# Optimization experiments

Hardware: AMD Instinct MI355X
Metric: run time of the kernel (lower is better)

The kernel has to match this reference:

```python
import jax, jax.numpy as jnp
import numpy as np

N, M, D = 384, 2, 3          # n_nodes, multiplicity, spatial dim
F, H, K, L = 32, 64, 2, 2    # feat dim, hidden, n_equivariant_vectors_out, n_blocks
OUT = 64                     # n_invariant_feat_out
T = N * M                    # flattened node count

def _edges():
    # fully-connected graph over flattened nodes, no self edges (static shapes)
    idx = np.arange(T)
    s = np.repeat(idx, T)
    r = np.tile(idx, T)
    mask = s != r
    return jnp.asarray(s[mask]), jnp.asarray(r[mask])

def setup_inputs() -> dict:
    key = jax.random.key(0)
    ks = jax.random.split(key, 12)
    def w(k, shape):
        return (jax.random.normal(k, shape) / np.sqrt(shape[-2])).astype(jnp.float32)
    return {
        "positions": jax.random.normal(ks[0], (N, M, D), dtype=jnp.float32),
        "features": jax.random.normal(ks[1], (N, M, F), dtype=jnp.float32),
        "w_emb": w(ks[2], (F, H)), "b_emb": jnp.zeros((H,), jnp.float32),
        "we1": w(ks[3], (L, 2 * H + K, H)), "be1": jnp.zeros((L, H), jnp.float32),
        "we2": w(ks[4], (L, H, H)), "be2": jnp.zeros((L, H), jnp.float32),
        "wx1": w(ks[5], (L, H, H)), "bx1": jnp.zeros((L, H), jnp.float32),
        "wx2": w(ks[6], (L, H, K)),
        "wh1": w(ks[7], (L, 2 * H, H)), "bh1": jnp.zeros((L, H), jnp.float32),
        "wh2": w(ks[8], (L, H, H)), "bh2": jnp.zeros((L, H), jnp.float32),
        "w_head": w(ks[9], (H, OUT)), "b_head": jnp.zeros((OUT,), jnp.float32),
    }

def reference(positions, features, w_emb, b_emb, we1, be1, we2, be2,
              wx1, bx1, wx2, wh1, bh1, wh2, bh2, w_head, b_head):
    senders, receivers = _edges()
    x = positions.reshape(T, D)                      # flatten multiplicity
    h = features.reshape(T, F) @ w_emb + b_emb       # [T,H] node embedding
    x_vec = jnp.repeat(x[:, None, :], K, axis=1)     # [T,K,3] vector channels
    for l in range(L):
        diff = x_vec[senders] - x_vec[receivers]                        # [E,K,3]
        sqnorm = jnp.sum(diff * diff, axis=-1)                          # [E,K]
        e_in = jnp.concatenate([h[senders], h[receivers], sqnorm], -1)  # [E,2H+K]
        m = jax.nn.silu(e_in @ we1[l] + be1[l])
        m = jax.nn.silu(m @ we2[l] + be2[l])                            # [E,H]
        phi_x = jax.nn.silu(m @ wx1[l] + bx1[l]) @ wx2[l]               # [E,K]
        upd = phi_x[..., None] * diff / (jnp.sqrt(sqnorm + 1e-8)[..., None] + 1.0)
        x_vec = x_vec + jax.ops.segment_sum(upd, receivers, num_segments=T) / (T - 1)
        agg = jax.ops.segment_sum(m, receivers, num_segments=T)         # [T,H]
        h = h + jax.nn.silu(jnp.concatenate([h, agg], -1) @ wh1[l] + bh1[l]) @ wh2[l] + bh2[l]
    vectors = (x_vec - x[:, None, :]).reshape(N, M, K, D)  # unflatten
    scalars = (h @ w_head + b_head).reshape(N, M, OUT)     # invariant head
    return vectors, scalars
```

## Files before the change

### kernel.cpp

```cpp
#include <hip/hip_runtime.h>
#include <math.h>

#define TN 768
#define HD 64
#define FF 32
#define OUTD 64
#define LL 2

typedef short short8 __attribute__((ext_vector_type(8)));
typedef short short4v __attribute__((ext_vector_type(4)));
typedef float f32x4 __attribute__((ext_vector_type(4)));
typedef unsigned int uint4v __attribute__((ext_vector_type(4)));

__device__ __forceinline__ float silu_f(float x) {
    float e = __builtin_amdgcn_exp2f(x * -1.44269504089f);
    return x * __builtin_amdgcn_rcpf(1.0f + e);
}

__device__ __forceinline__ void bf16_split(float x, short& hi, short& lo) {
    unsigned int u = __float_as_uint(x);
    unsigned int uh = u & 0xFFFF0000u;
    hi = (short)(uh >> 16);
    float r = x - __uint_as_float(uh);
    lo = (short)(__float_as_uint(r) >> 16);
}

__device__ __forceinline__ unsigned short bf16_rne(float x) {
    unsigned int u = __float_as_uint(x);
    u += 0x7FFFu + ((u >> 16) & 1u);
    return (unsigned short)(u >> 16);
}

__device__ __forceinline__ float row16_sum(float v) {
    int x;
    x = __builtin_amdgcn_update_dpp(0, __float_as_int(v), 0xB1, 0xF, 0xF, true);
    v += __int_as_float(x);
    x = __builtin_amdgcn_update_dpp(0, __float_as_int(v), 0x4E, 0xF, 0xF, true);
    v += __int_as_float(x);
    x = __builtin_amdgcn_update_dpp(0, __float_as_int(v), 0x141, 0xF, 0xF, true);
    v += __int_as_float(x);
    x = __builtin_amdgcn_update_dpp(0, __float_as_int(v), 0x140, 0xF, 0xF, true);
    v += __int_as_float(x);
    return v;
}

__global__ void k_embed_pre(const float* __restrict__ pos, const float* __restrict__ feat,
                            const float* __restrict__ w_emb, const float* __restrict__ b_emb,
                            const float* __restrict__ we1, const float* __restrict__ be1,
                            float* __restrict__ h, float* __restrict__ x_vec,
                            float* __restrict__ A, float* __restrict__ Bv) {
    int t = blockIdx.x;
    int j = threadIdx.x;
    __shared__ float sf[FF];
    __shared__ float sh[HD];
    if (j < FF) sf[j] = feat[t * FF + j];
    __syncthreads();
    float acc = b_emb[j];
#pragma unroll
    for (int f = 0; f < FF; ++f) acc += sf[f] * w_emb[f * HD + j];
    h[t * HD + j] = acc;
    sh[j] = acc;
    if (j < 6) x_vec[t * 6 + j] = pos[t * 3 + (j % 3)];
    __syncthreads();
    float a = be1[j], b = 0.f;
#pragma unroll
    for (int i = 0; i < HD; ++i) {
        a += sh[i] * we1[i * HD + j];
        b += sh[i] * we1[(HD + i) * HD + j];
    }
    A[t * HD + j] = a;
    Bv[t * HD + j] = b;
}

#define SM2S 68
__global__ __launch_bounds__(256, 1) void k_edge(
    const float* __restrict__ xv_in, const float* __restrict__ A_in,
    const float* __restrict__ Bv_in, const float* __restrict__ we1,
    const float* __restrict__ we2, const float* __restrict__ be2,
    const float* __restrict__ wx1, const float* __restrict__ bx1,
    const float* __restrict__ wx2,
    const float* __restrict__ wh1, const float* __restrict__ bh1,
    const float* __restrict__ wh2, const float* __restrict__ bh2,
    const float* __restrict__ be1,
    float* __restrict__ h, float* __restrict__ xv_out,
    float* __restrict__ A_out, float* __restrict__ Bv_out,
    const float* __restrict__ pos, const float* __restrict__ w_head,
    const float* __restrict__ b_head, float* __restrict__ out,
    int l, int last)
{
    const int r = blockIdx.x;
    const int tid = threadIdx.x;
    const int wv = tid >> 6;
    const int lane = tid & 63;
    const int q = lane >> 4;
    const int m = lane & 15;

    __shared__ __align__(16) union USm {
        struct {
            unsigned short W2h[64 * 72], W2l[64 * 72], W3h[64 * 72];
        } stg;
        struct {
            unsigned short M2[64 * SM2S];
            float Phi[64][2];
            float Agg[4][64];
            float XupW[4][8];
            float hr[64], aggF[64], su[64], h2[64];
        } run;
    } u;

    const float* w2 = we2 + (size_t)l * HD * HD;
    const float* w3 = wx1 + (size_t)l * HD * HD;
    for (int e = tid; e < HD * HD; e += 256) {
        int k = e >> 6, n = e & 63;
        short h16, l16;
        bf16_split(w2[e], h16, l16);
        u.stg.W2h[n * 72 + k] = (unsigned short)h16;
        u.stg.W2l[n * 72 + k] = (unsigned short)l16;
        u.stg.W3h[n * 72 + k] = bf16_rne(w3[e]);
    }
    __syncthreads();
    short8 bW2h[4][2], bW2l[4][2], bW3h[4][2];
#pragma unroll
    for (int nt = 0; nt < 4; ++nt)
#pragma unroll
        for (int kt = 0; kt < 2; ++kt) {
            int idx = (nt * 16 + m) * 72 + kt * 32 + 8 * q;
            bW2h[nt][kt] = *(const short8*)&u.stg.W2h[idx];
            bW2l[nt][kt] = *(const short8*)&u.stg.W2l[idx];
            bW3h[nt][kt] = *(const short8*)&u.stg.W3h[idx];
        }
    __syncthreads();

    float bbA[2][8], c0A[2][8], c1A[2][8];
#pragma unroll
    for (int kt = 0; kt < 2; ++kt) {
        int jb = kt * 32 + 8 * q;
        *(float4*)&bbA[kt][0] = *(const float4*)&Bv_in[r * HD + jb];
        *(float4*)&bbA[kt][4] = *(const float4*)&Bv_in[r * HD + jb + 4];
        *(float4*)&c0A[kt][0] = *(const float4*)&we1[((size_t)l * 130 + 128) * HD + jb];
        *(float4*)&c0A[kt][4] = *(const float4*)&we1[((size_t)l * 130 + 128) * HD + jb + 4];
        *(float4*)&c1A[kt][0] = *(const float4*)&we1[((size_t)l * 130 + 129) * HD + jb];
        *(float4*)&c1A[kt][4] = *(const float4*)&we1[((size_t)l * 130 + 129) * HD + jb + 4];
    }
    float be2v[4], bx1v[4], w20[4], w21[4];
#pragma unroll
    for (int nt = 0; nt < 4; ++nt) {
        int col = nt * 16 + m;
        be2v[nt] = be2[l * HD + col];
        bx1v[nt] = bx1[l * HD + col];
        w20[nt] = wx2[((size_t)l * HD + col) * 2 + 0];
        w21[nt] = wx2[((size_t)l * HD + col) * 2 + 1];
    }
    float xr[6];
#pragma unroll
    for (int c = 0; c < 6; ++c) xr[c] = xv_in[r * 6 + c];

    float aggP[4] = {0.f, 0.f, 0.f, 0.f};
    float accX[6] = {0.f, 0.f, 0.f, 0.f, 0.f, 0.f};

#pragma unroll 1
    for (int s0 = 0; s0 < TN; s0 += 64) {
        const int sA = s0 + 16 * wv + m;
        float2 p01 = *(const float2*)&xv_in[sA * 6 + 0];
        float2 p23 = *(const float2*)&xv_in[sA * 6 + 2];
        float2 p45 = *(const float2*)&xv_in[sA * 6 + 4];
        float d0 = p01.x - xr[0], d1 = p01.y - xr[1], d2 = p23.x - xr[2];
        float d3 = p23.y - xr[3], d4 = p45.x - xr[4], d5 = p45.y - xr[5];
        float q0 = d0 * d0 + d1 * d1 + d2 * d2;
        float q1 = d3 * d3 + d4 * d4 + d5 * d5;
        float ik0 = __builtin_amdgcn_rcpf(__builtin_amdgcn_sqrtf(q0 + 1e-8f) + 1.f);
        float ik1 = __builtin_amdgcn_rcpf(__builtin_amdgcn_sqrtf(q1 + 1e-8f) + 1.f);

        short8 a1h[2], a1l[2];
#pragma unroll
        for (int kt = 0; kt < 2; ++kt) {
            int jb = kt * 32 + 8 * q;
            float av[8];
            *(float4*)&av[0] = *(const float4*)&A_in[sA * HD + jb];
            *(float4*)&av[4] = *(const float4*)&A_in[sA * HD + jb + 4];
            float mv[8];
#pragma unroll
            for (int jj = 0; jj < 8; ++jj) {
                float pre = av[jj] + bbA[kt][jj] + q0 * c0A[kt][jj] + q1 * c1A[kt][jj];
                mv[jj] = silu_f(pre);
            }
            uint4v uh, ul;
            unsigned int* uhp = (unsigned int*)&uh;
            unsigned int* ulp = (unsigned int*)&ul;
#pragma unroll
            for (int jp = 0; jp < 4; ++jp) {
                unsigned int a0 = __float_as_uint(mv[2 * jp]);
                unsigned int a1 = __float_as_uint(mv[2 * jp + 1]);
                uhp[jp] = __builtin_amdgcn_perm(a1, a0, 0x07060302u);
                float l0 = mv[2 * jp] - __uint_as_float(a0 & 0xFFFF0000u);
                float l1 = mv[2 * jp + 1] - __uint_as_float(a1 & 0xFFFF0000u);
                ulp[jp] = __builtin_amdgcn_perm(__float_as_uint(l1), __float_as_uint(l0),
                                                0x07060302u);
            }
            a1h[kt] = __builtin_bit_cast(short8, uh);
            a1l[kt] = __builtin_bit_cast(short8, ul);
        }

        const int rl = r - s0;
#pragma unroll
        for (int nt = 0; nt < 4; ++nt) {
            f32x4 acc = {0.f, 0.f, 0.f, 0.f};
#pragma unroll
            for (int kt = 0; kt < 2; ++kt) {
                acc = __builtin_amdgcn_mfma_f32_16x16x32_bf16(a1h[kt], bW2h[nt][kt], acc, 0, 0, 0);
                acc = __builtin_amdgcn_mfma_f32_16x16x32_bf16(a1l[kt], bW2h[nt][kt], acc, 0, 0, 0);
                acc = __builtin_amdgcn_mfma_f32_16x16x32_bf16(a1h[kt], bW2l[nt][kt], acc, 0, 0, 0);
            }
            int col = nt * 16 + m;
#pragma unroll
            for (int reg = 0; reg < 4; ++reg) {
                int il = 16 * wv + 4 * q + reg;
                float v = silu_f(acc[reg] + be2v[nt]);
                if (il == rl) v = 0.f;
                aggP[nt] += v;
                u.run.M2[il * SM2S + col] = bf16_rne(v);
            }
        }

        short8 a2h[2];
#pragma unroll
        for (int kt = 0; kt < 2; ++kt) {
            int base = (16 * wv + m) * SM2S + kt * 32 + 8 * q;
            short4v lo = *(const short4v*)&u.run.M2[base];
            short4v hi = *(const short4v*)&u.run.M2[base + 4];
            short8 a2;
#pragma unroll
            for (int jj = 0; jj < 4; ++jj) { a2[jj] = lo[jj]; a2[4 + jj] = hi[jj]; }
            a2h[kt] = a2;
        }
        float phiP[4][2] = {};
#pragma unroll
        for (int nt = 0; nt < 4; ++nt) {
            f32x4 acc = {0.f, 0.f, 0.f, 0.f};
#pragma unroll
            for (int kt = 0; kt < 2; ++kt)
                acc = __builtin_amdgcn_mfma_f32_16x16x32_bf16(a2h[kt], bW3h[nt][kt], acc, 0, 0, 0);
#pragma unroll
            for (int reg = 0; reg < 4; ++reg) {
                float p = silu_f(acc[reg] + bx1v[nt]);
                phiP[reg][0] += p * w20[nt];
                phiP[reg][1] += p * w21[nt];
            }
        }
#pragma unroll
        for (int reg = 0; reg < 4; ++reg) {
            phiP[reg][0] = row16_sum(phiP[reg][0]);
            phiP[reg][1] = row16_sum(phiP[reg][1]);
        }
        if (m == 0) {
#pragma unroll
            for (int reg = 0; reg < 4; ++reg) {
                int il = 16 * wv + 4 * q + reg;
                *(float2*)&u.run.Phi[il][0] = make_float2(phiP[reg][0], phiP[reg][1]);
            }
        }
        if (q == 0) {
            int il = 16 * wv + m;
            float2 ph = *(const float2*)&u.run.Phi[il][0];
            float f0 = ph.x * ik0;
            float f1 = ph.y * ik1;
            accX[0] += f0 * d0; accX[1] += f0 * d1; accX[2] += f0 * d2;
            accX[3] += f1 * d3; accX[4] += f1 * d4; accX[5] += f1 * d5;
        }
    }

#pragma unroll
    for (int nt = 0; nt < 4; ++nt) {
        aggP[nt] += __shfl_xor(aggP[nt], 16, 64);
        aggP[nt] += __shfl_xor(aggP[nt], 32, 64);
    }
#pragma unroll
    for (int c = 0; c < 6; ++c) accX[c] = row16_sum(accX[c]);
    if (q == 0) {
#pragma unroll
        for (int nt = 0; nt < 4; ++nt) u.run.Agg[wv][nt * 16 + m] = aggP[nt];
        if (m == 0) {
#pragma unroll
            for (int c = 0; c < 6; ++c) u.run.XupW[wv][c] = accX[c];
        }
    }
    __syncthreads();

    float xup[6];
    if (tid < 64) {
        u.run.aggF[tid] = u.run.Agg[0][tid] + u.run.Agg[1][tid] +
                          u.run.Agg[2][tid] + u.run.Agg[3][tid];
        u.run.hr[tid] = h[r * HD + tid];
    }
    __syncthreads();
    if (tid < 64) {
        int j = tid;
        const float* w1 = wh1 + (size_t)l * 128 * HD;
        float acc = bh1[l * HD + j];
#pragma unroll
        for (int i = 0; i < HD; ++i) acc += u.run.hr[i] * w1[i * HD + j];
#pragma unroll
        for (int i = 0; i < HD; ++i) acc += u.run.aggF[i] * w1[(HD + i) * HD + j];
        u.run.su[j] = silu_f(acc);
    }
    __syncthreads();
    if (tid < 64) {
        int j = tid;
        const float* wq = wh2 + (size_t)l * HD * HD;
        float v = 0.f;
#pragma unroll
        for (int i = 0; i < HD; ++i) v += u.run.su[i] * wq[i * HD + j];
        float hn = u.run.hr[j] + v + bh2[l * HD + j];
        h[r * HD + j] = hn;
        u.run.h2[j] = hn;
    }
    if (tid < 6) {
        xup[0] = u.run.XupW[0][tid] + u.run.XupW[1][tid] +
                 u.run.XupW[2][tid] + u.run.XupW[3][tid];
    }
    __syncthreads();
    if (!last) {
        if (tid < 64) {
            int j = tid;
            const float* w = we1 + (size_t)(l + 1) * 130 * HD;
            float a = be1[(l + 1) * HD + j], b = 0.f;
#pragma unroll
            for (int i = 0; i < HD; ++i) {
                a += u.run.h2[i] * w[i * HD + j];
                b += u.run.h2[i] * w[(HD + i) * HD + j];
            }
            A_out[r * HD + j] = a;
            Bv_out[r * HD + j] = b;
        }
        if (tid < 6) {
            xv_out[r * 6 + tid] = xr[tid] + xup[0] * (1.0f / 767.0f);
        }
    } else {
        if (tid < 64) {
            int j = tid;
            float o = b_head[j];
#pragma unroll
            for (int i = 0; i < HD; ++i) o += u.run.h2[i] * w_head[i * OUTD + j];
            out[TN * 6 + r * OUTD + j] = o;
        }
        if (tid < 6) {
            float xv = xr[tid] + xup[0] * (1.0f / 767.0f);
            out[r * 6 + tid] = xv - pos[r * 3 + (tid % 3)];
        }
    }
}

extern "C" void kernel_launch(void* const* d_in, const int* in_sizes, int n_in,
                              void* d_out, int out_size, void* d_ws, size_t ws_size,
                              hipStream_t stream)
{
    const float* pos    = (const float*)d_in[0];
    const float* feat   = (const float*)d_in[1];
    const float* w_emb  = (const float*)d_in[2];
    const float* b_emb  = (const float*)d_in[3];
    const float* we1    = (const float*)d_in[4];
    const float* be1    = (const float*)d_in[5];
    const float* we2    = (const float*)d_in[6];
    const float* be2    = (const float*)d_in[7];
    const float* wx1    = (const float*)d_in[8];
    const float* bx1    = (const float*)d_in[9];
    const float* wx2    = (const float*)d_in[10];
    const float* wh1    = (const float*)d_in[11];
    const float* bh1    = (const float*)d_in[12];
    const float* wh2    = (const float*)d_in[13];
    const float* bh2    = (const float*)d_in[14];
    const float* w_head = (const float*)d_in[15];
    const float* b_head = (const float*)d_in[16];
    float* out = (float*)d_out;

    float* ws   = (float*)d_ws;
    float* h    = ws;
    float* xv0  = h + TN * HD;
    float* xv1  = xv0 + TN * 6;
    float* A0   = xv1 + TN * 6;
    float* A1   = A0 + TN * HD;
    float* Bv0  = A1 + TN * HD;
    float* Bv1  = Bv0 + TN * HD;

    k_embed_pre<<<TN, 64, 0, stream>>>(pos, feat, w_emb, b_emb, we1, be1,
                                       h, xv0, A0, Bv0);
    k_edge<<<TN, 256, 0, stream>>>(xv0, A0, Bv0, we1, we2, be2, wx1, bx1, wx2,
                                   wh1, bh1, wh2, bh2, be1,
                                   h, xv1, A1, Bv1,
                                   pos, w_head, b_head, out, 0, 0);
    k_edge<<<TN, 256, 0, stream>>>(xv1, A1, Bv1, we1, we2, be2, wx1, bx1, wx2,
                                   wh1, bh1, wh2, bh2, be1,
                                   h, xv0, A0, Bv0,
                                   pos, w_head, b_head, out, 1, 1);
}
```

Before: 211.3 us.

## Drop low-part bf16 split of first-layer activations and prefetch next sender tile

Removes the bf16 hi/lo split of the silu activations feeding the second edge MLP, cutting the MFMA count per tile from three to two per k-step and dropping the lo-part packing, and uses a packed bf16 convert instruction. Adds double-buffered register prefetch of the next 64 senders' positions and A rows so global loads overlap compute. Moves the per-receiver bias and sqnorm weight vectors into shared memory to lower register pressure, and takes the self-edge masking off the common path. The lower precision on the activation operand risks larger numerical error.

```diff
diff --git a/kernel.cpp b/kernel.cpp
--- a/kernel.cpp
+++ b/kernel.cpp
@@ -1,4 +1,5 @@
 #include <hip/hip_runtime.h>
+#include <hip/hip_bf16.h>
 #include <math.h>
 
 #define TN 768
@@ -29,6 +30,17 @@
     unsigned int u = __float_as_uint(x);
     u += 0x7FFFu + ((u >> 16) & 1u);
     return (unsigned short)(u >> 16);
+}
+
+__device__ __forceinline__ unsigned int pk_bf16(float a, float b) {
+#if __has_builtin(__builtin_amdgcn_cvt_pk_bf16_f32)
+    auto t = __builtin_amdgcn_cvt_pk_bf16_f32(a, b);
+    return __builtin_bit_cast(unsigned int, t);
+#else
+    unsigned int ua = __float_as_uint(a); ua += 0x7FFFu + ((ua >> 16) & 1u);
+    unsigned int ub = __float_as_uint(b); ub += 0x7FFFu + ((ub >> 16) & 1u);
+    return __builtin_amdgcn_perm(ub, ua, 0x07060302u);
+#endif
 }
 
 __device__ __forceinline__ float row16_sum(float v) {
@@ -107,6 +119,9 @@
             float hr[64], aggF[64], su[64], h2[64];
         } run;
     } u;
+    __shared__ __align__(16) float sBvr[64];
+    __shared__ __align__(16) float sC0[64];
+    __shared__ __align__(16) float sC1[64];
 
     const float* w2 = we2 + (size_t)l * HD * HD;
     const float* w3 = wx1 + (size_t)l * HD * HD;
@@ -118,6 +133,11 @@
         u.stg.W2l[n * 72 + k] = (unsigned short)l16;
         u.stg.W3h[n * 72 + k] = bf16_rne(w3[e]);
     }
+    if (tid < HD) {
+        sBvr[tid] = Bv_in[r * HD + tid];
+        sC0[tid] = we1[((size_t)l * 130 + 128) * HD + tid];
+        sC1[tid] = we1[((size_t)l * 130 + 129) * HD + tid];
+    }
     __syncthreads();
     short8 bW2h[4][2], bW2l[4][2], bW3h[4][2];
 #pragma unroll
@@ -131,17 +151,6 @@
         }
     __syncthreads();
 
-    float bbA[2][8], c0A[2][8], c1A[2][8];
-#pragma unroll
-    for (int kt = 0; kt < 2; ++kt) {
-        int jb = kt * 32 + 8 * q;
-        *(float4*)&bbA[kt][0] = *(const float4*)&Bv_in[r * HD + jb];
-        *(float4*)&bbA[kt][4] = *(const float4*)&Bv_in[r * HD + jb + 4];
-        *(float4*)&c0A[kt][0] = *(const float4*)&we1[((size_t)l * 130 + 128) * HD + jb];
-        *(float4*)&c0A[kt][4] = *(const float4*)&we1[((size_t)l * 130 + 128) * HD + jb + 4];
-        *(float4*)&c1A[kt][0] = *(const float4*)&we1[((size_t)l * 130 + 129) * HD + jb];
-        *(float4*)&c1A[kt][4] = *(const float4*)&we1[((size_t)l * 130 + 129) * HD + jb + 4];
-    }
     float be2v[4], bx1v[4], w20[4], w21[4];
 #pragma unroll
     for (int nt = 0; nt < 4; ++nt) {
@@ -158,12 +167,37 @@
     float aggP[4] = {0.f, 0.f, 0.f, 0.f};
     float accX[6] = {0.f, 0.f, 0.f, 0.f, 0.f, 0.f};
 
-#pragma unroll 1
-    for (int s0 = 0; s0 < TN; s0 += 64) {
-        const int sA = s0 + 16 * wv + m;
-        float2 p01 = *(const float2*)&xv_in[sA * 6 + 0];
-        float2 p23 = *(const float2*)&xv_in[sA * 6 + 2];
-        float2 p45 = *(const float2*)&xv_in[sA * 6 + 4];
+    const int rowA = 16 * wv + m;
+    float2 pbuf[2][3];
+    float4 abuf[2][2][2];
+    {
+        int sA = rowA;
+        pbuf[0][0] = *(const float2*)&xv_in[sA * 6 + 0];
+        pbuf[0][1] = *(const float2*)&xv_in[sA * 6 + 2];
+        pbuf[0][2] = *(const float2*)&xv_in[sA * 6 + 4];
+#pragma unroll
+        for (int kt = 0; kt < 2; ++kt) {
+            abuf[0][kt][0] = *(const float4*)&A_in[sA * HD + kt * 32 + 8 * q];
+            abuf[0][kt][1] = *(const float4*)&A_in[sA * HD + kt * 32 + 8 * q + 4];
+        }
+    }
+
+#pragma unroll 2
+    for (int it = 0; it < TN / 64; ++it) {
+        const int s0 = it * 64;
+        const int pb = it & 1;
+        {
+            int sN = (s0 + 64 < TN ? s0 + 64 : 0) + rowA;
+            pbuf[pb ^ 1][0] = *(const float2*)&xv_in[sN * 6 + 0];
+            pbuf[pb ^ 1][1] = *(const float2*)&xv_in[sN * 6 + 2];
+            pbuf[pb ^ 1][2] = *(const float2*)&xv_in[sN * 6 + 4];
+#pragma unroll
+            for (int kt = 0; kt < 2; ++kt) {
+                abuf[pb ^ 1][kt][0] = *(const float4*)&A_in[sN * HD + kt * 32 + 8 * q];
+                abuf[pb ^ 1][kt][1] = *(const float4*)&A_in[sN * HD + kt * 32 + 8 * q + 4];
+            }
+        }
+        float2 p01 = pbuf[pb][0], p23 = pbuf[pb][1], p45 = pbuf[pb][2];
         float d0 = p01.x - xr[0], d1 = p01.y - xr[1], d2 = p23.x - xr[2];
         float d3 = p23.y - xr[3], d4 = p45.x - xr[4], d5 = p45.y - xr[5];
         float q0 = d0 * d0 + d1 * d1 + d2 * d2;
@@ -171,61 +205,68 @@
         float ik0 = __builtin_amdgcn_rcpf(__builtin_amdgcn_sqrtf(q0 + 1e-8f) + 1.f);
         float ik1 = __builtin_amdgcn_rcpf(__builtin_amdgcn_sqrtf(q1 + 1e-8f) + 1.f);
 
-        short8 a1h[2], a1l[2];
+        short8 a1h[2];
 #pragma unroll
         for (int kt = 0; kt < 2; ++kt) {
             int jb = kt * 32 + 8 * q;
-            float av[8];
-            *(float4*)&av[0] = *(const float4*)&A_in[sA * HD + jb];
-            *(float4*)&av[4] = *(const float4*)&A_in[sA * HD + jb + 4];
+            float av[8], bb[8], c0[8], c1[8];
+            *(float4*)&av[0] = abuf[pb][kt][0];
+            *(float4*)&av[4] = abuf[pb][kt][1];
+            *(float4*)&bb[0] = *(const float4*)&sBvr[jb];
+            *(float4*)&bb[4] = *(const float4*)&sBvr[jb + 4];
+            *(float4*)&c0[0] = *(const float4*)&sC0[jb];
+            *(float4*)&c0[4] = *(const float4*)&sC0[jb + 4];
+            *(float4*)&c1[0] = *(const float4*)&sC1[jb];
+            *(float4*)&c1[4] = *(const float4*)&sC1[jb + 4];
             float mv[8];
 #pragma unroll
             for (int jj = 0; jj < 8; ++jj) {
-                float pre = av[jj] + bbA[kt][jj] + q0 * c0A[kt][jj] + q1 * c1A[kt][jj];
+                float pre = av[jj] + bb[jj] + q0 * c0[jj] + q1 * c1[jj];
                 mv[jj] = silu_f(pre);
             }
-            uint4v uh, ul;
+            uint4v uh;
             unsigned int* uhp = (unsigned int*)&uh;
-            unsigned int* ulp = (unsigned int*)&ul;
-#pragma unroll
-            for (int jp = 0; jp < 4; ++jp) {
-                unsigned int a0 = __float_as_uint(mv[2 * jp]);
-                unsigned int a1 = __float_as_uint(mv[2 * jp + 1]);
-                uhp[jp] = __builtin_amdgcn_perm(a1, a0, 0x07060302u);
-                float l0 = mv[2 * jp] - __uint_as_float(a0 & 0xFFFF0000u);
-                float l1 = mv[2 * jp + 1] - __uint_as_float(a1 & 0xFFFF0000u);
-                ulp[jp] = __builtin_amdgcn_perm(__float_as_uint(l1), __float_as_uint(l0),
-                                                0x07060302u);
-            }
+#pragma unroll
+            for (int jp = 0; jp < 4; ++jp)
+                uhp[jp] = pk_bf16(mv[2 * jp], mv[2 * jp + 1]);
             a1h[kt] = __builtin_bit_cast(short8, uh);
-            a1l[kt] = __builtin_bit_cast(short8, ul);
         }
 
         const int rl = r - s0;
+        const bool selfw = (rl >= 16 * wv) && (rl < 16 * wv + 16);
 #pragma unroll
         for (int nt = 0; nt < 4; ++nt) {
             f32x4 acc = {0.f, 0.f, 0.f, 0.f};
 #pragma unroll
             for (int kt = 0; kt < 2; ++kt) {
                 acc = __builtin_amdgcn_mfma_f32_16x16x32_bf16(a1h[kt], bW2h[nt][kt], acc, 0, 0, 0);
-                acc = __builtin_amdgcn_mfma_f32_16x16x32_bf16(a1l[kt], bW2h[nt][kt], acc, 0, 0, 0);
                 acc = __builtin_amdgcn_mfma_f32_16x16x32_bf16(a1h[kt], bW2l[nt][kt], acc, 0, 0, 0);
             }
-            int col = nt * 16 + m;
-#pragma unroll
-            for (int reg = 0; reg < 4; ++reg) {
-                int il = 16 * wv + 4 * q + reg;
-                float v = silu_f(acc[reg] + be2v[nt]);
-                if (il == rl) v = 0.f;
-                aggP[nt] += v;
-                u.run.M2[il * SM2S + col] = bf16_rne(v);
-            }
+            float vv[4];
+#pragma unroll
+            for (int reg = 0; reg < 4; ++reg) vv[reg] = silu_f(acc[reg] + be2v[nt]);
+            const int il0 = 16 * wv + 4 * q;
+            if (__builtin_expect(selfw, 0)) {
+#pragma unroll
+                for (int reg = 0; reg < 4; ++reg)
+                    aggP[nt] += (il0 + reg == rl) ? 0.f : vv[reg];
+            } else {
+#pragma unroll
+                for (int reg = 0; reg < 4; ++reg) aggP[nt] += vv[reg];
+            }
+            const int col = nt * 16 + m;
+            unsigned int pA = pk_bf16(vv[0], vv[1]);
+            unsigned int pB = pk_bf16(vv[2], vv[3]);
+            u.run.M2[(il0 + 0) * SM2S + col] = (unsigned short)pA;
+            u.run.M2[(il0 + 1) * SM2S + col] = (unsigned short)(pA >> 16);
+            u.run.M2[(il0 + 2) * SM2S + col] = (unsigned short)pB;
+            u.run.M2[(il0 + 3) * SM2S + col] = (unsigned short)(pB >> 16);
         }
 
         short8 a2h[2];
 #pragma unroll
         for (int kt = 0; kt < 2; ++kt) {
-            int base = (16 * wv + m) * SM2S + kt * 32 + 8 * q;
+            int base = rowA * SM2S + kt * 32 + 8 * q;
             short4v lo = *(const short4v*)&u.run.M2[base];
             short4v hi = *(const short4v*)&u.run.M2[base + 4];
             short8 a2;
@@ -260,8 +301,7 @@
             }
         }
         if (q == 0) {
-            int il = 16 * wv + m;
-            float2 ph = *(const float2*)&u.run.Phi[il][0];
+            float2 ph = *(const float2*)&u.run.Phi[rowA][0];
             float f0 = ph.x * ik0;
             float f1 = ph.y * ik1;
             accX[0] += f0 * d0; accX[1] += f0 * d1; accX[2] += f0 * d2;
@@ -286,7 +326,7 @@
     }
     __syncthreads();
 
-    float xup[6];
+    float xup = 0.f;
     if (tid < 64) {
         u.run.aggF[tid] = u.run.Agg[0][tid] + u.run.Agg[1][tid] +
                           u.run.Agg[2][tid] + u.run.Agg[3][tid];
@@ -315,8 +355,8 @@
         u.run.h2[j] = hn;
     }
     if (tid < 6) {
-        xup[0] = u.run.XupW[0][tid] + u.run.XupW[1][tid] +
-                 u.run.XupW[2][tid] + u.run.XupW[3][tid];
+        xup = u.run.XupW[0][tid] + u.run.XupW[1][tid] +
+              u.run.XupW[2][tid] + u.run.XupW[3][tid];
     }
     __syncthreads();
     if (!last) {
@@ -333,7 +373,7 @@
             Bv_out[r * HD + j] = b;
         }
         if (tid < 6) {
-            xv_out[r * 6 + tid] = xr[tid] + xup[0] * (1.0f / 767.0f);
+            xv_out[r * 6 + tid] = xr[tid] + xup * (1.0f / 767.0f);
         }
     } else {
         if (tid < 64) {
@@ -344,7 +384,7 @@
             out[TN * 6 + r * OUTD + j] = o;
         }
         if (tid < 6) {
-            float xv = xr[tid] + xup[0] * (1.0f / 767.0f);
+            float xv = xr[tid] + xup * (1.0f / 767.0f);
             out[r * 6 + tid] = xv - pos[r * 3 + (tid % 3)];
         }
     }
```

After: 239.8 us. 1.13x slower.
